# Kernel tuning notes

Measured on AMD Instinct MI355X. Metric: run time of the kernel, lower is better.

The kernel has to match this reference:

```python
import jax, jax.numpy as jnp
import numpy as np

BETA = 0.25
DECAY = 0.99
EPS = 1e-05
N_E = 1024
E_DIM = 64

def setup_inputs() -> dict:
    key = jax.random.key(0)
    k1, k2, k3, k4 = jax.random.split(key, 4)
    z = jax.random.normal(k1, (32, 64, 32, 32), dtype=jnp.float32)
    embedding = jax.random.normal(k2, (N_E, E_DIM), dtype=jnp.float32)
    cluster_size = jax.random.uniform(k3, (N_E,), dtype=jnp.float32)
    cluster_sum = jax.random.normal(k4, (N_E, E_DIM), dtype=jnp.float32)
    return {"z": z, "embedding": embedding, "cluster_size": cluster_size, "cluster_sum": cluster_sum}


def reference(z, embedding, cluster_size, cluster_sum):
    # z: (B, C, H, W) with C == e_dim
    zp = jnp.transpose(z, (0, 2, 3, 1))            # (B, H, W, C)
    zf = zp.reshape(-1, E_DIM)                      # (N, e_dim)
    # squared-distance matrix: ||z||^2 + ||e||^2 - 2 z.e  -> (N, n_e)
    distance = (jnp.sum(zf ** 2, axis=1, keepdims=True)
                + jnp.sum(embedding ** 2, axis=1)
                - 2.0 * (zf @ embedding.T))
    idx = jnp.argmin(distance, axis=1)              # (N,)
    # one-hot counts / cluster sums expressed as segment sums (same math)
    counts = jax.ops.segment_sum(jnp.ones(zf.shape[0], dtype=zf.dtype), idx, num_segments=N_E)
    sums = jax.ops.segment_sum(zf, idx, num_segments=N_E)
    # EMA buffer update (module is in training mode -> embedding refreshed)
    new_cluster_size = DECAY * cluster_size + (1.0 - DECAY) * counts
    new_cluster_sum = DECAY * cluster_sum + (1.0 - DECAY) * sums
    new_embed = new_cluster_sum / (new_cluster_size + EPS)[:, None]
    z_q = new_embed[idx].reshape(zp.shape)          # gather-dequantize
    L_commitment = jnp.mean((jax.lax.stop_gradient(z_q) - zp) ** 2)
    loss = BETA * L_commitment
    z_q = zp + jax.lax.stop_gradient(z_q - zp)      # straight-through
    z_q = jnp.transpose(z_q, (0, 3, 1, 2))          # back to (B, C, H, W)
    return z_q, loss, counts
```

## Files before the change

### kernel.cpp

```cpp
#include <hip/hip_runtime.h>
#include <hip/hip_bf16.h>


#define N_ROWS   32768
#define N_CODES  1024
#define EDIM     64
#define ZQ_ELEMS 2097152

__global__ void vq_enorm(const float* __restrict__ emb, float* __restrict__ enorm) {
    int c = blockIdx.x * 256 + threadIdx.x;
    if (c < N_CODES) {
        float s = 0.f;
        #pragma unroll
        for (int k = 0; k < EDIM; ++k) {
            float v = emb[(c << 6) + k];
            s = fmaf(v, v, s);
        }
        enorm[c] = s;
    }
}

__global__ __launch_bounds__(256, 2) void vq_dist(
        const float* __restrict__ z, const float* __restrict__ emb,
        const float* __restrict__ enorm,
        int* __restrict__ idx_out, float* __restrict__ counts,
        float* __restrict__ sums) {
    __shared__ float zT[64 * 68];
    __shared__ float eT[64 * 128];
    __shared__ float znorm_s[64];
    __shared__ float enorm_s[128];
    __shared__ int   idx_s[64];

    const int t   = threadIdx.x;
    const int r0  = blockIdx.x * 64;
    const int b   = r0 >> 10;
    const int hw0 = r0 & 1023;

    {
        const int row = t & 63, q = t >> 6;
        #pragma unroll
        for (int i = 0; i < 16; ++i) {
            const int c = i * 4 + q;
            zT[c * 68 + row] = z[((b * 64 + c) << 10) + hw0 + row];
        }
    }
    __syncthreads();

    if (t < 64) {
        float s = 0.f;
        #pragma unroll
        for (int k = 0; k < EDIM; ++k) {
            const float v = zT[k * 68 + t];
            s = fmaf(v, v, s);
        }
        znorm_s[t] = s;
    }
    __syncthreads();

    const int tx = t & 15, ty = t >> 4;
    const int row0 = ty * 4;
    const int cA = tx * 4, cB = 64 + tx * 4;

    float zn[4];
    #pragma unroll
    for (int r = 0; r < 4; ++r) zn[r] = znorm_s[row0 + r];

    float best[4] = {INFINITY, INFINITY, INFINITY, INFINITY};
    int   bidx[4] = {0, 0, 0, 0};

    for (int ch = 0; ch < 8; ++ch) {
        #pragma unroll
        for (int p = 0; p < 8; ++p) {
            const int li = p * 1024 + t * 4;
            const int cl = li >> 6, k4 = li & 63;
            const float4 v = *(const float4*)&emb[((ch * 128 + cl) << 6) + k4];
            eT[(k4 + 0) * 128 + cl] = v.x;
            eT[(k4 + 1) * 128 + cl] = v.y;
            eT[(k4 + 2) * 128 + cl] = v.z;
            eT[(k4 + 3) * 128 + cl] = v.w;
        }
        if (t < 128) enorm_s[t] = enorm[ch * 128 + t];
        __syncthreads();

        float acc[4][8];
        #pragma unroll
        for (int r = 0; r < 4; ++r)
            #pragma unroll
            for (int j = 0; j < 8; ++j) acc[r][j] = 0.f;

        #pragma unroll 4
        for (int k = 0; k < 64; ++k) {
            const float4 zv = *(const float4*)&zT[k * 68 + row0];
            const float4 ea = *(const float4*)&eT[k * 128 + cA];
            const float4 eb = *(const float4*)&eT[k * 128 + cB];
            const float za[4] = {zv.x, zv.y, zv.z, zv.w};
            const float e8[8] = {ea.x, ea.y, ea.z, ea.w, eb.x, eb.y, eb.z, eb.w};
            #pragma unroll
            for (int r = 0; r < 4; ++r)
                #pragma unroll
                for (int j = 0; j < 8; ++j)
                    acc[r][j] = fmaf(za[r], e8[j], acc[r][j]);
        }

        #pragma unroll
        for (int r = 0; r < 4; ++r) {
            #pragma unroll
            for (int j = 0; j < 8; ++j) {
                const int cl = (j < 4) ? (cA + j) : (cB + (j - 4));
                const float s = (zn[r] + enorm_s[cl]) - 2.0f * acc[r][j];
                if (s < best[r]) { best[r] = s; bidx[r] = ch * 128 + cl; }
            }
        }
        __syncthreads();
    }

    #pragma unroll
    for (int off = 1; off < 16; off <<= 1) {
        #pragma unroll
        for (int r = 0; r < 4; ++r) {
            const float os = __shfl_xor(best[r], off);
            const int   oi = __shfl_xor(bidx[r], off);
            if (os < best[r] || (os == best[r] && oi < bidx[r])) {
                best[r] = os; bidx[r] = oi;
            }
        }
    }
    if (tx == 0) {
        #pragma unroll
        for (int r = 0; r < 4; ++r) {
            const int row = row0 + r;
            idx_out[r0 + row] = bidx[r];
            atomicAdd(&counts[bidx[r]], 1.0f);
            idx_s[row] = bidx[r];
        }
    }
    __syncthreads();

    {
        const int k = t & 63, q = t >> 6;
        #pragma unroll
        for (int i = 0; i < 16; ++i) {
            const int row = i * 4 + q;
            atomicAdd(&sums[idx_s[row] * 64 + k], zT[k * 68 + row]);
        }
    }
}

__global__ void vq_ema(const float* __restrict__ counts, const float* __restrict__ sums,
                       const float* __restrict__ cs, const float* __restrict__ csum,
                       float* __restrict__ new_embed, float* __restrict__ out_counts,
                       float* __restrict__ out_loss) {
    const int g = blockIdx.x * 256 + threadIdx.x;
    const int c = g >> 6, d = g & 63;
    const float cnt = counts[c];
    const float nsize = 0.99f * cs[c] + 0.01f * cnt;
    const float nsum  = 0.99f * csum[g] + 0.01f * sums[g];
    new_embed[g] = nsum / (nsize + 1e-5f);
    if (d == 0) out_counts[c] = cnt;
    if (g == 0) out_loss[0] = 0.f;
}

__global__ __launch_bounds__(256) void vq_gather(
        const float* __restrict__ z, const int* __restrict__ idx,
        const float* __restrict__ new_embed,
        float* __restrict__ out_zq, float* __restrict__ out_loss) {
    __shared__ float red[4];
    const int t = threadIdx.x;
    const int r0 = blockIdx.x * 256;
    const int b  = r0 >> 10;
    const int hw = (r0 & 1023) + t;
    const int myidx = idx[r0 + t];

    float lsum = 0.f;
    #pragma unroll 8
    for (int c = 0; c < 64; ++c) {
        const float e  = new_embed[(myidx << 6) + c];
        const int  off = ((b * 64 + c) << 10) + hw;
        const float zv = z[off];
        const float diff = e - zv;
        out_zq[off] = zv + diff;
        lsum = fmaf(diff, diff, lsum);
    }
    #pragma unroll
    for (int off = 32; off >= 1; off >>= 1) lsum += __shfl_down(lsum, off);
    if ((t & 63) == 0) red[t >> 6] = lsum;
    __syncthreads();
    if (t == 0) {
        const float s = red[0] + red[1] + red[2] + red[3];
        atomicAdd(out_loss, s * (0.25f / 2097152.0f));
    }
}

extern "C" void kernel_launch(void* const* d_in, const int* in_sizes, int n_in,
                              void* d_out, int out_size, void* d_ws, size_t ws_size,
                              hipStream_t stream) {
    const float* z    = (const float*)d_in[0];
    const float* emb  = (const float*)d_in[1];
    const float* cs   = (const float*)d_in[2];
    const float* csum = (const float*)d_in[3];
    float* out = (float*)d_out;

    int*   idx       = (int*)d_ws;
    float* counts    = (float*)d_ws + 32768;
    float* sums      = counts + 1024;
    float* enorm     = sums + 65536;
    float* new_embed = enorm + 1024;

    hipMemsetAsync(counts, 0, (1024 + 65536) * sizeof(float), stream);

    vq_enorm<<<4, 256, 0, stream>>>(emb, enorm);
    vq_dist<<<512, 256, 0, stream>>>(z, emb, enorm, idx, counts, sums);
    vq_ema<<<256, 256, 0, stream>>>(counts, sums, cs, csum, new_embed,
                                    out + ZQ_ELEMS + 1,
                                    out + ZQ_ELEMS);
    vq_gather<<<128, 256, 0, stream>>>(z, idx, new_embed, out, out + ZQ_ELEMS);
}
```

Before: 173.8 us.

## Restructure distance kernel to per-row registers with wave-split codebook search

The distance kernel drops the shared-memory register-tiled GEMM. Each thread now holds one z row (64 floats) in registers, and each of the 8 waves scans 128 codes, reading embeddings directly from global memory (a wave-uniform broadcast). Per-wave minima are then reduced through shared memory, and the block is enlarged to 512 threads. The gather kernel also preloads each row's embedding into registers with float4 loads. The aim is to remove LDS staging and syncs, but each thread now gives up register-tile reuse and does many scalar global or scalar-cache loads per FMA, and register pressure is high.

New measurement: 329.7 us. +89.8%, slower.

```diff
diff --git a/kernel.cpp b/kernel.cpp
--- a/kernel.cpp
+++ b/kernel.cpp
@@ -20,129 +20,77 @@
     }
 }
 
-__global__ __launch_bounds__(256, 2) void vq_dist(
+__global__ __launch_bounds__(512, 2) void vq_dist(
         const float* __restrict__ z, const float* __restrict__ emb,
         const float* __restrict__ enorm,
         int* __restrict__ idx_out, float* __restrict__ counts,
         float* __restrict__ sums) {
-    __shared__ float zT[64 * 68];
-    __shared__ float eT[64 * 128];
-    __shared__ float znorm_s[64];
-    __shared__ float enorm_s[128];
-    __shared__ int   idx_s[64];
+    __shared__ float zs[64 * 65];
+    __shared__ float best_s[8 * 64];
+    __shared__ int   bidx_s[8 * 64];
+    __shared__ int   idx_sh[64];
 
-    const int t   = threadIdx.x;
-    const int r0  = blockIdx.x * 64;
-    const int b   = r0 >> 10;
-    const int hw0 = r0 & 1023;
+    const int t    = threadIdx.x;
+    const int lane = t & 63;
+    const int wv   = t >> 6;
+    const int r0   = blockIdx.x * 64;
+    const int b    = r0 >> 10;
+    const int hw0  = r0 & 1023;
 
-    {
-        const int row = t & 63, q = t >> 6;
-        #pragma unroll
-        for (int i = 0; i < 16; ++i) {
-            const int c = i * 4 + q;
-            zT[c * 68 + row] = z[((b * 64 + c) << 10) + hw0 + row];
-        }
+    #pragma unroll
+    for (int i = 0; i < 8; ++i) {
+        const int c = wv + 8 * i;
+        zs[lane * 65 + c] = z[((b * 64 + c) << 10) + hw0 + lane];
     }
     __syncthreads();
 
-    if (t < 64) {
-        float s = 0.f;
+    float zr[64];
+    #pragma unroll
+    for (int k = 0; k < EDIM; ++k) zr[k] = zs[lane * 65 + k];
+
+    float zn = 0.f;
+    #pragma unroll
+    for (int k = 0; k < EDIM; ++k) zn = fmaf(zr[k], zr[k], zn);
+
+    float best = INFINITY;
+    int   bidx = 0;
+    const int c0 = wv * 128;
+    for (int c = c0; c < c0 + 128; c += 2) {
+        const float* __restrict__ e0 = emb + (c << 6);
+        float a0 = 0.f, a1 = 0.f;
         #pragma unroll
         for (int k = 0; k < EDIM; ++k) {
-            const float v = zT[k * 68 + t];
-            s = fmaf(v, v, s);
+            a0 = fmaf(zr[k], e0[k], a0);
+            a1 = fmaf(zr[k], e0[EDIM + k], a1);
         }
-        znorm_s[t] = s;
+        const float s0 = (zn + enorm[c]) - 2.0f * a0;
+        const float s1 = (zn + enorm[c + 1]) - 2.0f * a1;
+        if (s0 < best) { best = s0; bidx = c; }
+        if (s1 < best) { best = s1; bidx = c + 1; }
+    }
+    best_s[wv * 64 + lane] = best;
+    bidx_s[wv * 64 + lane] = bidx;
+    __syncthreads();
+
+    if (t < 64) {
+        float bb = best_s[t];
+        int   bi = bidx_s[t];
+        #pragma unroll
+        for (int w = 1; w < 8; ++w) {
+            const float ob = best_s[w * 64 + t];
+            const int   oi = bidx_s[w * 64 + t];
+            if (ob < bb) { bb = ob; bi = oi; }
+        }
+        idx_out[r0 + t] = bi;
+        idx_sh[t] = bi;
+        atomicAdd(&counts[bi], 1.0f);
     }
     __syncthreads();
 
-    const int tx = t & 15, ty = t >> 4;
-    const int row0 = ty * 4;
-    const int cA = tx * 4, cB = 64 + tx * 4;
-
-    float zn[4];
     #pragma unroll
-    for (int r = 0; r < 4; ++r) zn[r] = znorm_s[row0 + r];
-
-    float best[4] = {INFINITY, INFINITY, INFINITY, INFINITY};
-    int   bidx[4] = {0, 0, 0, 0};
-
-    for (int ch = 0; ch < 8; ++ch) {
-        #pragma unroll
-        for (int p = 0; p < 8; ++p) {
-            const int li = p * 1024 + t * 4;
-            const int cl = li >> 6, k4 = li & 63;
-            const float4 v = *(const float4*)&emb[((ch * 128 + cl) << 6) + k4];
-            eT[(k4 + 0) * 128 + cl] = v.x;
-            eT[(k4 + 1) * 128 + cl] = v.y;
-            eT[(k4 + 2) * 128 + cl] = v.z;
-            eT[(k4 + 3) * 128 + cl] = v.w;
-        }
-        if (t < 128) enorm_s[t] = enorm[ch * 128 + t];
-        __syncthreads();
-
-        float acc[4][8];
-        #pragma unroll
-        for (int r = 0; r < 4; ++r)
-            #pragma unroll
-            for (int j = 0; j < 8; ++j) acc[r][j] = 0.f;
-
-        #pragma unroll 4
-        for (int k = 0; k < 64; ++k) {
-            const float4 zv = *(const float4*)&zT[k * 68 + row0];
-            const float4 ea = *(const float4*)&eT[k * 128 + cA];
-            const float4 eb = *(const float4*)&eT[k * 128 + cB];
-            const float za[4] = {zv.x, zv.y, zv.z, zv.w};
-            const float e8[8] = {ea.x, ea.y, ea.z, ea.w, eb.x, eb.y, eb.z, eb.w};
-            #pragma unroll
-            for (int r = 0; r < 4; ++r)
-                #pragma unroll
-                for (int j = 0; j < 8; ++j)
-                    acc[r][j] = fmaf(za[r], e8[j], acc[r][j]);
-        }
-
-        #pragma unroll
-        for (int r = 0; r < 4; ++r) {
-            #pragma unroll
-            for (int j = 0; j < 8; ++j) {
-                const int cl = (j < 4) ? (cA + j) : (cB + (j - 4));
-                const float s = (zn[r] + enorm_s[cl]) - 2.0f * acc[r][j];
-                if (s < best[r]) { best[r] = s; bidx[r] = ch * 128 + cl; }
-            }
-        }
-        __syncthreads();
-    }
-
-    #pragma unroll
-    for (int off = 1; off < 16; off <<= 1) {
-        #pragma unroll
-        for (int r = 0; r < 4; ++r) {
-            const float os = __shfl_xor(best[r], off);
-            const int   oi = __shfl_xor(bidx[r], off);
-            if (os < best[r] || (os == best[r] && oi < bidx[r])) {
-                best[r] = os; bidx[r] = oi;
-            }
-        }
-    }
-    if (tx == 0) {
-        #pragma unroll
-        for (int r = 0; r < 4; ++r) {
-            const int row = row0 + r;
-            idx_out[r0 + row] = bidx[r];
-            atomicAdd(&counts[bidx[r]], 1.0f);
-            idx_s[row] = bidx[r];
-        }
-    }
-    __syncthreads();
-
-    {
-        const int k = t & 63, q = t >> 6;
-        #pragma unroll
-        for (int i = 0; i < 16; ++i) {
-            const int row = i * 4 + q;
-            atomicAdd(&sums[idx_s[row] * 64 + k], zT[k * 68 + row]);
-        }
+    for (int i = 0; i < 8; ++i) {
+        const int row = i * 8 + wv;
+        atomicAdd(&sums[idx_sh[row] * 64 + lane], zs[row * 65 + lane]);
     }
 }
 
@@ -165,16 +113,21 @@
         const float* __restrict__ new_embed,
         float* __restrict__ out_zq, float* __restrict__ out_loss) {
     __shared__ float red[4];
-    const int t = threadIdx.x;
+    const int t  = threadIdx.x;
     const int r0 = blockIdx.x * 256;
     const int b  = r0 >> 10;
     const int hw = (r0 & 1023) + t;
     const int myidx = idx[r0 + t];
 
+    const float4* __restrict__ er = (const float4*)(new_embed + (myidx << 6));
+    float4 e4[16];
+    #pragma unroll
+    for (int i = 0; i < 16; ++i) e4[i] = er[i];
+
     float lsum = 0.f;
-    #pragma unroll 8
+    #pragma unroll
     for (int c = 0; c < 64; ++c) {
-        const float e  = new_embed[(myidx << 6) + c];
+        const float e  = ((const float*)e4)[c];
         const int  off = ((b * 64 + c) << 10) + hw;
         const float zv = z[off];
         const float diff = e - zv;
@@ -209,7 +162,7 @@
     hipMemsetAsync(counts, 0, (1024 + 65536) * sizeof(float), stream);
 
     vq_enorm<<<4, 256, 0, stream>>>(emb, enorm);
-    vq_dist<<<512, 256, 0, stream>>>(z, emb, enorm, idx, counts, sums);
+    vq_dist<<<512, 512, 0, stream>>>(z, emb, enorm, idx, counts, sums);
     vq_ema<<<256, 256, 0, stream>>>(counts, sums, cs, csum, new_embed,
                                     out + ZQ_ELEMS + 1,
                                     out + ZQ_ELEMS);
```
